# Performance work log

Hardware: AMD Instinct MI355X
Metric: run time of the kernel (lower is better)

## Reference

```python
import jax, jax.numpy as jnp
import numpy as np

B, N, T, F, H, NH, E, R = 16, 100, 96, 26, 128, 4, 16, 8


def _ln(x, g, b, eps=1e-5):
    m = x.mean(-1, keepdims=True)
    v = ((x - m) ** 2).mean(-1, keepdims=True)
    return (x - m) / jnp.sqrt(v + eps) * g + b


def setup_inputs() -> dict:
    ks = iter(jax.random.split(jax.random.key(0), 64))

    def nrm(*shape):
        return jax.random.normal(next(ks), shape, jnp.float32) * 0.05

    z = lambda *s: jnp.zeros(s, jnp.float32)
    o = lambda *s: jnp.ones(s, jnp.float32)
    inp = {}
    inp['x'] = jax.random.normal(next(ks), (B, N, T, F), jnp.float32)
    A = jax.random.uniform(next(ks), (N, N), jnp.float32)
    inp['A_norm'] = A / A.sum(1, keepdims=True)
    inp['H_inc'] = (jax.random.uniform(next(ks), (N, E)) > 0.7).astype(jnp.float32).at[:, 0].set(1.0)
    inp['membership'] = jax.random.randint(next(ks), (N,), 0, R)
    inp['Wp'] = nrm(H, F); inp['bp'] = z(H)
    inp['g_p'] = o(H); inp['b_p'] = z(H)
    inp['Wqkv'] = nrm(3 * H, H); inp['bqkv'] = z(3 * H)
    inp['Wo'] = nrm(H, H); inp['bo'] = z(H)
    inp['g_a'] = o(H); inp['b_a'] = z(H)
    inp['Wih_f'] = nrm(4 * H, H); inp['Whh_f'] = nrm(4 * H, H)
    inp['bih_f'] = z(4 * H); inp['bhh_f'] = z(4 * H)
    inp['Wih_b'] = nrm(4 * H, H); inp['Whh_b'] = nrm(4 * H, H)
    inp['bih_b'] = z(4 * H); inp['bhh_b'] = z(4 * H)
    inp['Wtp'] = nrm(H, 2 * H); inp['btp'] = z(H)
    inp['Wn'] = nrm(H, H); inp['bn'] = z(H)
    inp['We'] = nrm(H, H); inp['be'] = z(H)
    inp['Wa'] = nrm(1, H); inp['ba'] = z(1)
    inp['g_g'] = o(H); inp['b_g'] = z(H)
    inp['Remb'] = nrm(R, H)
    inp['Wg'] = nrm(H, H); inp['bg'] = z(H)
    inp['Wf'] = nrm(H, 2 * H); inp['bf'] = z(H)
    inp['g_f'] = o(H); inp['b_f'] = z(H)
    inp['W1'] = nrm(H // 2, H); inp['b1'] = z(H // 2)
    inp['W2'] = nrm(1, H // 2); inp['b2'] = z(1)
    return inp


def reference(x, A_norm, H_inc, membership, Wp, bp, g_p, b_p, Wqkv, bqkv, Wo, bo,
              g_a, b_a, Wih_f, Whh_f, bih_f, bhh_f, Wih_b, Whh_b, bih_b, bhh_b,
              Wtp, btp, Wn, bn, We, be, Wa, ba, g_g, b_g, Remb, Wg, bg,
              Wf, bf, g_f, b_f, W1, b1, W2, b2):
    B_, N_, T_, F_ = x.shape
    H_ = Wp.shape[0]
    BN = B_ * N_
    # input_proj (dropout = identity in eval)
    h = jax.nn.relu(_ln(x.reshape(BN, T_, F_) @ Wp.T + bp, g_p, b_p))
    # temporal multi-head self-attention + residual + LN
    qkv = h @ Wqkv.T + bqkv
    q, k, v = jnp.split(qkv, 3, -1)
    dh = H_ // NH
    sh = lambda t: t.reshape(BN, T_, NH, dh).transpose(0, 2, 1, 3)
    q, k, v = sh(q), sh(k), sh(v)
    att = jax.nn.softmax(jnp.einsum('bhqd,bhkd->bhqk', q, k) / jnp.sqrt(jnp.float32(dh)), -1)
    ao = jnp.einsum('bhqk,bhkd->bhqd', att, v).transpose(0, 2, 1, 3).reshape(BN, T_, H_)
    h = _ln(ao @ Wo.T + bo + h, g_a, b_a)
    # bidirectional LSTM (PyTorch gate order i,f,g,o), take t = T-1
    def lstm_scan(seq, Wih, Whh, bih, bhh):
        def step(carry, xt):
            hp, cp = carry
            gates = xt @ Wih.T + bih + hp @ Whh.T + bhh
            i, f, g, o_ = jnp.split(gates, 4, -1)
            c = jax.nn.sigmoid(f) * cp + jax.nn.sigmoid(i) * jnp.tanh(g)
            hn = jax.nn.sigmoid(o_) * jnp.tanh(c)
            return (hn, c), hn
        z0 = jnp.zeros((seq.shape[1], H_), seq.dtype)
        _, ys = jax.lax.scan(step, (z0, z0), seq)
        return ys
    seq = h.transpose(1, 0, 2)  # (T, BN, H)
    y_f = lstm_scan(seq, Wih_f, Whh_f, bih_f, bhh_f)[-1]        # fwd hidden at t=T-1
    y_b = lstm_scan(seq[::-1], Wih_b, Whh_b, bih_b, bhh_b)[0]   # bwd hidden at t=T-1
    h_temporal = (jnp.concatenate([y_f, y_b], -1) @ Wtp.T + btp).reshape(B_, N_, H_)
    # spatial: HyperGAT (segment softmax over incident hyperedges) + GCN + region emb
    mask = H_inc > 0                        # (N, E)
    deg_e = H_inc.sum(0)                    # (E,)
    has_edge = mask.any(-1, keepdims=True)  # (N, 1)
    r_emb = Remb[membership]                # (N, H)

    def spatial(hb):
        npj = hb @ Wn.T + bn
        ee = (H_inc.T @ npj) / (deg_e[:, None] + 1e-8)
        ee = ee @ We.T + be                 # (E, H)
        sc = (ee @ Wa.T + ba)[:, 0]         # (E,)
        w = jax.nn.softmax(jnp.where(mask, sc[None, :], -1e9), -1)
        w = jnp.where(has_edge, w, 0.0)
        hb2 = _ln(w @ ee + hb, g_g, b_g)
        hg = jax.nn.relu((A_norm @ hb2) @ Wg.T + bg)
        return hb2 + hg + r_emb

    h_spatial = jax.vmap(spatial)(h_temporal)
    h_fused = jax.nn.relu(_ln(jnp.concatenate([h_temporal, h_spatial], -1) @ Wf.T + bf, g_f, b_f))
    pred = (jax.nn.relu(h_fused @ W1.T + b1) @ W2.T + b2)[..., 0]
    return pred, h_spatial, h_temporal
```

## Files before the change

### kernel.cpp

```cpp
#include <hip/hip_runtime.h>
#include <hip/hip_bf16.h>

typedef __hip_bfloat16 bf16;
typedef __attribute__((ext_vector_type(8))) short bf8v;
typedef __attribute__((ext_vector_type(4))) short s4v;
typedef __attribute__((ext_vector_type(4))) float f4v;

#define DEV __device__ __forceinline__

DEV float b2f(bf16 v){ return __bfloat162float(v); }
DEV bf16 f2b(float v){ return __float2bfloat16(v); }
DEV short f2bs(float v){ bf16 t = __float2bfloat16(v); return *reinterpret_cast<short*>(&t); }
DEV float s2f(short s){ return __uint_as_float(((unsigned int)(unsigned short)s) << 16); }
DEV float blo(unsigned int u){ return __uint_as_float(u << 16); }
DEV float bhi(unsigned int u){ return __uint_as_float(u & 0xffff0000u); }
DEV float rcpf_(float x){ return __builtin_amdgcn_rcpf(x); }
DEV float sigf(float x){ return rcpf_(1.0f + __expf(-x)); }
DEV float tanhfast(float x){
  x = fminf(fmaxf(x, -15.0f), 15.0f);
  float e = __expf(-2.0f*x);
  return (1.0f - e)*rcpf_(1.0f + e);
}

DEV f4v mfma16(bf8v a, bf8v b, f4v c){
  return __builtin_amdgcn_mfma_f32_16x16x32_bf16(a, b, c, 0, 0, 0);
}

DEV float ln128(float s, int tid, const bf16* g, const bf16* b, float* red){
  float sum = s, sq = s*s;
  #pragma unroll
  for (int off = 32; off; off >>= 1){
    sum += __shfl_down(sum, off);
    sq  += __shfl_down(sq,  off);
  }
  if ((tid & 63) == 0){ red[(tid>>6)*2] = sum; red[(tid>>6)*2+1] = sq; }
  __syncthreads();
  float S = red[0] + red[2], Q = red[1] + red[3];
  float m  = S * (1.0f/128.0f);
  float var = fmaxf(Q * (1.0f/128.0f) - m*m, 0.0f);
  float rs = rsqrtf(var + 1e-5f);
  float y = (s - m)*rs*b2f(g[tid]) + b2f(b[tid]);
  __syncthreads();
  return y;
}

__global__ void k_detect(const unsigned int* __restrict__ xw, int* __restrict__ flag){
  __shared__ int found;
  if (threadIdx.x == 0) found = 0;
  __syncthreads();
  int local = 0;
  for (int i = threadIdx.x; i < 4096; i += 256){
    unsigned int u = xw[i];
    unsigned int e = (u >> 7) & 0xFF;
    if (e >= 0x90) local = 1;
  }
  if (local) atomicOr(&found, 1);
  __syncthreads();
  if (threadIdx.x == 0) flag[0] = found ? 0 : 1;
}

struct CArgs {
  const void* src[44];
  int n[44];
  int off[44];
};

__global__ void k_canon(CArgs a, const int* __restrict__ flag, bf16* __restrict__ dst){
  int id = blockIdx.y;
  int n = a.n[id];
  const void* s = a.src[id];
  bf16* d = dst + a.off[id];
  int stride = gridDim.x * blockDim.x;
  int i0 = blockIdx.x * blockDim.x + threadIdx.x;
  if (flag[0]){
    const bf16* sb = (const bf16*)s;
    for (int i = i0; i < n; i += stride) d[i] = sb[i];
  } else {
    const float* sf = (const float*)s;
    for (int i = i0; i < n; i += stride) d[i] = f2b(sf[i]);
  }
}

__global__ void k_inproj(const bf16* __restrict__ x, const bf16* __restrict__ Wp,
                         const bf16* __restrict__ bp, const bf16* __restrict__ gp,
                         const bf16* __restrict__ bbp, bf16* __restrict__ h0){
  int row0 = blockIdx.x*8, tid = threadIdx.x;
  __shared__ float xs[8*26];
  __shared__ float red[4];
  float wreg[26];
  #pragma unroll
  for (int f = 0; f < 26; ++f) wreg[f] = b2f(Wp[tid*26 + f]);
  float bias = b2f(bp[tid]);
  for (int i = tid; i < 208; i += 128) xs[i] = b2f(x[row0*26 + i]);
  __syncthreads();
  for (int r = 0; r < 8; ++r){
    float s = bias;
    #pragma unroll
    for (int f = 0; f < 26; ++f) s += xs[r*26 + f]*wreg[f];
    float y = fmaxf(ln128(s, tid, gp, bbp, red), 0.0f);
    h0[(row0 + r)*128 + tid] = f2b(y);
  }
}

__global__ __launch_bounds__(256,1) void k_attn(const bf16* __restrict__ h0,
    const bf16* __restrict__ Wqkv, const bf16* __restrict__ bqkv,
    bf16* __restrict__ attno){
  int bn = blockIdx.x;
  int tid = threadIdx.x;
  int w = tid >> 6;
  int lane = tid & 63;
  int l15 = lane & 15, quad = lane >> 4;

  __shared__ __align__(16) short h0s[96*136];
  __shared__ __align__(16) short q_sh[4][96*40];
  __shared__ __align__(16) short k_sh[4][96*40];
  __shared__ __align__(16) short v_sh[4][32*104];

  {
    const uint4* src = (const uint4*)(h0 + bn*12288);
    uint4* dst = (uint4*)h0s;
    for (int u = tid; u < 1536; u += 256){
      int r = u >> 4, c = u & 15;
      dst[r*17 + c] = src[u];
    }
  }
  __syncthreads();

  short* qp = q_sh[w];
  short* kp = k_sh[w];
  short* vp = v_sh[w];
  const float scl = 0.17677669529663687f;

  #pragma unroll
  for (int pan = 0; pan < 3; ++pan){
    for (int n0 = 0; n0 < 32; n0 += 16){
      int rq = pan*128 + w*32 + n0 + l15;
      bf8v b[4];
      #pragma unroll
      for (int ksi = 0; ksi < 4; ++ksi)
        b[ksi] = *reinterpret_cast<const bf8v*>(Wqkv + rq*128 + ksi*32 + quad*8);
      float bias = b2f(bqkv[rq]);
      for (int m = 0; m < 6; ++m){
        f4v acc = {0.f,0.f,0.f,0.f};
        #pragma unroll
        for (int ksi = 0; ksi < 4; ++ksi){
          bf8v a = *reinterpret_cast<const bf8v*>(h0s + (m*16 + l15)*136 + ksi*32 + quad*8);
          acc = mfma16(a, b[ksi], acc);
        }
        if (pan == 0){
          #pragma unroll
          for (int r = 0; r < 4; ++r)
            qp[(m*16 + quad*4 + r)*40 + n0 + l15] = f2bs((acc[r] + bias)*scl);
        } else if (pan == 1){
          #pragma unroll
          for (int r = 0; r < 4; ++r)
            kp[(m*16 + quad*4 + r)*40 + n0 + l15] = f2bs(acc[r] + bias);
        } else {
          s4v vs;
          #pragma unroll
          for (int r = 0; r < 4; ++r) vs[r] = f2bs(acc[r] + bias);
          *reinterpret_cast<s4v*>(vp + (n0 + l15)*104 + m*16 + quad*4) = vs;
        }
      }
    }
  }
  __syncthreads();

  short* pp = h0s + w*1664;

  for (int m = 0; m < 6; ++m){
    bf8v aq = *reinterpret_cast<const bf8v*>(qp + (m*16 + l15)*40 + quad*8);
    f4v s[6];
    #pragma unroll
    for (int n = 0; n < 6; ++n){
      bf8v bk = *reinterpret_cast<const bf8v*>(kp + (n*16 + l15)*40 + quad*8);
      f4v z = {0.f,0.f,0.f,0.f};
      s[n] = mfma16(aq, bk, z);
    }
    float mr[4], sr[4];
    #pragma unroll
    for (int r = 0; r < 4; ++r){
      float m0 = fmaxf(fmaxf(s[0][r], s[1][r]), fmaxf(s[2][r], s[3][r]));
      mr[r] = fmaxf(m0, fmaxf(s[4][r], s[5][r]));
    }
    #pragma unroll
    for (int mask = 1; mask < 16; mask <<= 1)
      #pragma unroll
      for (int r = 0; r < 4; ++r) mr[r] = fmaxf(mr[r], __shfl_xor(mr[r], mask));
    #pragma unroll
    for (int r = 0; r < 4; ++r) sr[r] = 0.0f;
    #pragma unroll
    for (int n = 0; n < 6; ++n)
      #pragma unroll
      for (int r = 0; r < 4; ++r){
        float p = __expf(s[n][r] - mr[r]);
        s[n][r] = p;
        sr[r] += p;
      }
    #pragma unroll
    for (int mask = 1; mask < 16; mask <<= 1)
      #pragma unroll
      for (int r = 0; r < 4; ++r) sr[r] += __shfl_xor(sr[r], mask);
    #pragma unroll
    for (int n = 0; n < 6; ++n)
      #pragma unroll
      for (int r = 0; r < 4; ++r)
        pp[(quad*4 + r)*104 + n*16 + l15] = f2bs(s[n][r]);
    asm volatile("s_waitcnt lgkmcnt(0)" ::: "memory");
    f4v o0 = {0.f,0.f,0.f,0.f}, o1 = {0.f,0.f,0.f,0.f};
    #pragma unroll
    for (int ksi = 0; ksi < 3; ++ksi){
      bf8v ap  = *reinterpret_cast<const bf8v*>(pp + l15*104 + ksi*32 + quad*8);
      bf8v bv0 = *reinterpret_cast<const bf8v*>(vp + l15*104 + ksi*32 + quad*8);
      bf8v bv1 = *reinterpret_cast<const bf8v*>(vp + (16 + l15)*104 + ksi*32 + quad*8);
      o0 = mfma16(ap, bv0, o0);
      o1 = mfma16(ap, bv1, o1);
    }
    #pragma unroll
    for (int r = 0; r < 4; ++r){
      float inv = 1.0f/sr[r];
      int row = bn*96 + m*16 + quad*4 + r;
      attno[row*128 + w*32 + l15]      = f2b(o0[r]*inv);
      attno[row*128 + w*32 + 16 + l15] = f2b(o1[r]*inv);
    }
  }
}

__global__ __launch_bounds__(256,1) void k_oproj(const bf16* __restrict__ attno,
    const bf16* __restrict__ h0, const bf16* __restrict__ Wo,
    const bf16* __restrict__ bo, const bf16* __restrict__ ga,
    const bf16* __restrict__ ba_, bf16* __restrict__ h1){
  int rt = blockIdx.x;
  int tid = threadIdx.x;
  int w = tid >> 6, lane = tid & 63;
  int l15 = lane & 15, quad = lane >> 4;
  __shared__ __align__(16) short atile[128*136];
  {
    const uint4* src = (const uint4*)(attno + rt*16384);
    uint4* dst = (uint4*)atile;
    for (int u = tid; u < 2048; u += 256){
      int r = u >> 4, c = u & 15;
      dst[r*17 + c] = src[u];
    }
  }
  __syncthreads();
  int m0 = w*32;
  bf8v a[2][4];
  #pragma unroll
  for (int m = 0; m < 2; ++m)
    #pragma unroll
    for (int ksi = 0; ksi < 4; ++ksi)
      a[m][ksi] = *reinterpret_cast<const bf8v*>(atile + (m0 + m*16 + l15)*136 + ksi*32 + quad*8);
  f4v acc[2][8];
  #pragma unroll
  for (int m = 0; m < 2; ++m)
    #pragma unroll
    for (int n = 0; n < 8; ++n) acc[m][n] = (f4v){0.f,0.f,0.f,0.f};
  for (int n = 0; n < 8; ++n){
    int G = n*16 + l15;
    bf8v b[4];
    #pragma unroll
    for (int ksi = 0; ksi < 4; ++ksi)
      b[ksi] = *reinterpret_cast<const bf8v*>(Wo + G*128 + ksi*32 + quad*8);
    #pragma unroll
    for (int m = 0; m < 2; ++m)
      #pragma unroll
      for (int ksi = 0; ksi < 4; ++ksi)
        acc[m][n] = mfma16(a[m][ksi], b[ksi], acc[m][n]);
  }
  #pragma unroll
  for (int m = 0; m < 2; ++m){
    int rowbase = rt*128 + m0 + m*16;
    #pragma unroll
    for (int n = 0; n < 8; ++n){
      int col = n*16 + l15;
      float bia = b2f(bo[col]);
      #pragma unroll
      for (int r = 0; r < 4; ++r)
        acc[m][n][r] += bia + b2f(h0[(rowbase + quad*4 + r)*128 + col]);
    }
    float sm[4], sq[4];
    #pragma unroll
    for (int r = 0; r < 4; ++r){ sm[r] = 0.f; sq[r] = 0.f; }
    #pragma unroll
    for (int n = 0; n < 8; ++n)
      #pragma unroll
      for (int r = 0; r < 4; ++r){
        float v = acc[m][n][r];
        sm[r] += v; sq[r] += v*v;
      }
    #pragma unroll
    for (int mask = 1; mask < 16; mask <<= 1)
      #pragma unroll
      for (int r = 0; r < 4; ++r){
        sm[r] += __shfl_xor(sm[r], mask);
        sq[r] += __shfl_xor(sq[r], mask);
      }
    float mean[4], rs[4];
    #pragma unroll
    for (int r = 0; r < 4; ++r){
      mean[r] = sm[r]*(1.0f/128.0f);
      float var = fmaxf(sq[r]*(1.0f/128.0f) - mean[r]*mean[r], 0.0f);
      rs[r] = rsqrtf(var + 1e-5f);
    }
    #pragma unroll
    for (int n = 0; n < 8; ++n){
      int col = n*16 + l15;
      float gv = b2f(ga[col]), bv = b2f(ba_[col]);
      #pragma unroll
      for (int r = 0; r < 4; ++r){
        float y = (acc[m][n][r] - mean[r])*rs[r]*gv + bv;
        h1[(rowbase + quad*4 + r)*128 + col] = f2b(y);
      }
    }
  }
}

__global__ __launch_bounds__(512,1) void k_lstm(const bf16* __restrict__ Whh,
    const bf16* __restrict__ Wih, const bf16* __restrict__ bih,
    const bf16* __restrict__ bhh, const bf16* __restrict__ h1,
    float* __restrict__ y_f){
  int bn0 = blockIdx.x * 16;
  int tid = threadIdx.x;
  int w = tid >> 6, lane = tid & 63;
  int l15 = lane & 15, quad = lane >> 4;
  __shared__ __align__(16) short hbuf[2][16*136];
  __shared__ __align__(16) short xbuf[2][16*136];

  bf8v whh[4][4], wih[4][4];
  float bias[4];
  #pragma unroll
  for (int role = 0; role < 4; ++role){
    int G = role*128 + w*16 + l15;
    #pragma unroll
    for (int kt = 0; kt < 4; ++kt){
      whh[role][kt] = *reinterpret_cast<const bf8v*>(Whh + G*128 + kt*32 + quad*8);
      wih[role][kt] = *reinterpret_cast<const bf8v*>(Wih + G*128 + kt*32 + quad*8);
    }
    bias[role] = b2f(bih[G]) + b2f(bhh[G]);
  }
  for (int i = tid; i < 16*136; i += 512) hbuf[0][i] = 0;
  if (tid < 256){
    const uint4* h1u4 = (const uint4*)h1;
    int row = (bn0 + (tid >> 4))*96 + 0;
    ((uint4*)xbuf[0])[(tid >> 4)*17 + (tid & 15)] = h1u4[row*16 + (tid & 15)];
  }
  f4v c0 = {0.f,0.f,0.f,0.f};
  __syncthreads();

  for (int t = 0; t < 96; ++t){
    int cur = t & 1, nxt = cur ^ 1;
    uint4 xpre;
    if (t < 95 && tid < 256){
      const uint4* h1u4 = (const uint4*)h1;
      int row = (bn0 + (tid >> 4))*96 + t + 1;
      xpre = h1u4[row*16 + (tid & 15)];
    }
    bf8v ah[4], ax[4];
    #pragma unroll
    for (int kt = 0; kt < 4; ++kt){
      ah[kt] = *reinterpret_cast<const bf8v*>(hbuf[cur] + l15*136 + kt*32 + quad*8);
      ax[kt] = *reinterpret_cast<const bf8v*>(xbuf[cur] + l15*136 + kt*32 + quad*8);
    }
    f4v acc[4];
    #pragma unroll
    for (int role = 0; role < 4; ++role){
      f4v z = {0.f,0.f,0.f,0.f};
      #pragma unroll
      for (int kt = 0; kt < 4; ++kt) z = mfma16(ax[kt], wih[role][kt], z);
      #pragma unroll
      for (int kt = 0; kt < 4; ++kt) z = mfma16(ah[kt], whh[role][kt], z);
      acc[role] = z;
    }
    float hreg[4];
    #pragma unroll
    for (int r = 0; r < 4; ++r){
      float i_ = acc[0][r] + bias[0];
      float f_ = acc[1][r] + bias[1];
      float g_ = acc[2][r] + bias[2];
      float o_ = acc[3][r] + bias[3];
      float c  = sigf(f_)*c0[r] + sigf(i_)*tanhfast(g_);
      hreg[r]  = sigf(o_)*tanhfast(c);
      c0[r] = c;
    }
    #pragma unroll
    for (int r = 0; r < 4; ++r)
      hbuf[nxt][(quad*4 + r)*136 + w*16 + l15] = f2bs(hreg[r]);
    if (t < 95 && tid < 256)
      ((uint4*)xbuf[nxt])[(tid >> 4)*17 + (tid & 15)] = xpre;
    __syncthreads();
  }
  for (int idx = tid; idx < 2048; idx += 512){
    int r = idx >> 7, d = idx & 127;
    y_f[(bn0 + r)*128 + d] = s2f(hbuf[0][r*136 + d]);
  }
}

__global__ void k_bwdtp(const bf16* __restrict__ h1, const bf16* __restrict__ Wihb,
                        const bf16* __restrict__ bihb, const bf16* __restrict__ bhhb,
                        const float* __restrict__ y_f, const bf16* __restrict__ Wtp,
                        const bf16* __restrict__ btp, float* __restrict__ ht,
                        const int* __restrict__ flag, bf16* __restrict__ outb,
                        float* __restrict__ outf){
  int bn = blockIdx.x, tid = threadIdx.x;
  __shared__ __align__(16) float xr[128];
  __shared__ float gates[512];
  __shared__ __align__(16) float ycat[256];
  xr[tid] = b2f(h1[(bn*96 + 95)*128 + tid]);
  __syncthreads();
  const float2* xf2 = (const float2*)xr;
  for (int g = tid; g < 512; g += 128){
    const unsigned int* w = (const unsigned int*)(Wihb + g*128);
    float s = b2f(bihb[g]) + b2f(bhhb[g]);
    #pragma unroll 8
    for (int kp = 0; kp < 64; ++kp){
      float2 a = xf2[kp]; unsigned int u = w[kp];
      s += a.x*blo(u) + a.y*bhi(u);
    }
    gates[g] = s;
  }
  __syncthreads();
  float ii = gates[tid], gg = gates[256 + tid], oo = gates[384 + tid];
  float c  = sigf(ii)*tanhfast(gg);
  float yb = sigf(oo)*tanhfast(c);
  ycat[tid]       = y_f[bn*128 + tid];
  ycat[128 + tid] = yb;
  __syncthreads();
  const float2* yf2 = (const float2*)ycat;
  const unsigned int* w = (const unsigned int*)(Wtp + tid*256);
  float s = b2f(btp[tid]);
  #pragma unroll 8
  for (int kp = 0; kp < 128; ++kp){
    float2 a = yf2[kp]; unsigned int u = w[kp];
    s += a.x*blo(u) + a.y*bhi(u);
  }
  ht[bn*128 + tid] = s;
  int oi = 206400 + bn*128 + tid;
  if (flag[0]) outb[oi] = f2b(s); else outf[oi] = s;
}

__global__ void k_npj(const float* __restrict__ ht, const bf16* __restrict__ Wn,
                      const bf16* __restrict__ bn_, float* __restrict__ npj){
  int bn = blockIdx.x, tid = threadIdx.x;
  __shared__ __align__(16) float row[128];
  row[tid] = ht[bn*128 + tid];
  __syncthreads();
  const float2* rf2 = (const float2*)row;
  const unsigned int* w = (const unsigned int*)(Wn + tid*128);
  float s = b2f(bn_[tid]);
  #pragma unroll 8
  for (int kp = 0; kp < 64; ++kp){
    float2 a = rf2[kp]; unsigned int u = w[kp];
    s += a.x*blo(u) + a.y*bhi(u);
  }
  npj[bn*128 + tid] = s;
}

__global__ void k_edge(const float* __restrict__ npj, const bf16* __restrict__ Hinc,
                       const bf16* __restrict__ We, const bf16* __restrict__ be,
                       const bf16* __restrict__ Wa, const bf16* __restrict__ ba,
                       float* __restrict__ ee, float* __restrict__ scE){
  int b = blockIdx.x >> 4, e = blockIdx.x & 15, tid = threadIdx.x;
  float acc = 0.0f, deg = 0.0f;
  for (int n = 0; n < 100; ++n){
    float w = b2f(Hinc[n*16 + e]);
    deg += w;
    acc += w * npj[(b*100 + n)*128 + tid];
  }
  __shared__ __align__(16) float eep[128];
  eep[tid] = acc/(deg + 1e-8f);
  __syncthreads();
  const float2* ef2 = (const float2*)eep;
  const unsigned int* w = (const unsigned int*)(We + tid*128);
  float s = b2f(be[tid]);
  #pragma unroll 8
  for (int kp = 0; kp < 64; ++kp){
    float2 a = ef2[kp]; unsigned int u = w[kp];
    s += a.x*blo(u) + a.y*bhi(u);
  }
  ee[(b*16 + e)*128 + tid] = s;
  float p = s * b2f(Wa[tid]);
  #pragma unroll
  for (int off = 32; off; off >>= 1) p += __shfl_down(p, off);
  __shared__ float r2[2];
  if ((tid & 63) == 0) r2[tid>>6] = p;
  __syncthreads();
  if (tid == 0) scE[b*16 + e] = r2[0] + r2[1] + b2f(ba[0]);
}

__global__ void k_node(const float* __restrict__ ht, const float* __restrict__ ee,
                       const float* __restrict__ scE, const bf16* __restrict__ Hinc,
                       const bf16* __restrict__ gg_, const bf16* __restrict__ bg_,
                       float* __restrict__ hb2){
  int blk = blockIdx.x; int b = blk/100, n = blk%100; int tid = threadIdx.x;
  __shared__ float wts[16];
  __shared__ float red[4];
  if (tid == 0){
    float sc[16]; float mx = -1e30f;
    for (int e = 0; e < 16; ++e){
      float m_ = b2f(Hinc[n*16 + e]);
      sc[e] = (m_ > 0.0f) ? scE[b*16 + e] : -1e30f;
      mx = fmaxf(mx, sc[e]);
    }
    float tmp[16]; float sum = 0.0f;
    for (int e = 0; e < 16; ++e){
      tmp[e] = (sc[e] > -1e29f) ? __expf(sc[e] - mx) : 0.0f;
      sum += tmp[e];
    }
    float inv = (sum > 0.0f) ? 1.0f/sum : 0.0f;
    for (int e = 0; e < 16; ++e) wts[e] = tmp[e]*inv;
  }
  __syncthreads();
  float s = ht[(b*100 + n)*128 + tid];
  for (int e = 0; e < 16; ++e) s += wts[e] * ee[(b*16 + e)*128 + tid];
  float y = ln128(s, tid, gg_, bg_, red);
  hb2[(b*100 + n)*128 + tid] = y;
}

__global__ void k_gcn(const float* __restrict__ hb2, const bf16* __restrict__ An,
                      const bf16* __restrict__ Wg, const bf16* __restrict__ bg_,
                      const bf16* __restrict__ Remb, const int* __restrict__ mem,
                      float* __restrict__ hsp, const int* __restrict__ flag,
                      bf16* __restrict__ outb, float* __restrict__ outf){
  int blk = blockIdx.x; int b = blk/100, n = blk%100; int tid = threadIdx.x;
  float acc = 0.0f;
  for (int m = 0; m < 100; ++m){
    float a = b2f(An[n*100 + m]);
    acc += a * hb2[(b*100 + m)*128 + tid];
  }
  __shared__ __align__(16) float as_[128];
  as_[tid] = acc;
  __syncthreads();
  const float2* af2 = (const float2*)as_;
  const unsigned int* w = (const unsigned int*)(Wg + tid*128);
  float s = b2f(bg_[tid]);
  #pragma unroll 8
  for (int kp = 0; kp < 64; ++kp){
    float2 a = af2[kp]; unsigned int u = w[kp];
    s += a.x*blo(u) + a.y*bhi(u);
  }
  s = fmaxf(s, 0.0f);
  float out = hb2[(b*100 + n)*128 + tid] + s + b2f(Remb[mem[n]*128 + tid]);
  hsp[(b*100 + n)*128 + tid] = out;
  int oi = 1600 + (b*100 + n)*128 + tid;
  if (flag[0]) outb[oi] = f2b(out); else outf[oi] = out;
}

__global__ void k_fuse(const float* __restrict__ ht, const float* __restrict__ hsp,
                       const bf16* __restrict__ Wf, const bf16* __restrict__ bf_,
                       const bf16* __restrict__ gf, const bf16* __restrict__ b_f,
                       const bf16* __restrict__ W1, const bf16* __restrict__ b1,
                       const bf16* __restrict__ W2, const bf16* __restrict__ b2,
                       const int* __restrict__ flag, bf16* __restrict__ outb,
                       float* __restrict__ outf){
  int bn = blockIdx.x, tid = threadIdx.x;
  __shared__ __align__(16) float cat[256];
  __shared__ __align__(16) float hf[128];
  __shared__ float red[4];
  cat[tid]       = ht[bn*128 + tid];
  cat[128 + tid] = hsp[bn*128 + tid];
  __syncthreads();
  const float2* cf2 = (const float2*)cat;
  const unsigned int* w = (const unsigned int*)(Wf + tid*256);
  float s = b2f(bf_[tid]);
  #pragma unroll 8
  for (int kp = 0; kp < 128; ++kp){
    float2 a = cf2[kp]; unsigned int u = w[kp];
    s += a.x*blo(u) + a.y*bhi(u);
  }
  float y = fmaxf(ln128(s, tid, gf, b_f, red), 0.0f);
  hf[tid] = y;
  __syncthreads();
  if (tid < 64){
    const float2* hf2 = (const float2*)hf;
    const unsigned int* w1 = (const unsigned int*)(W1 + tid*128);
    float z = b2f(b1[tid]);
    #pragma unroll 8
    for (int kp = 0; kp < 64; ++kp){
      float2 a = hf2[kp]; unsigned int u = w1[kp];
      z += a.x*blo(u) + a.y*bhi(u);
    }
    z = fmaxf(z, 0.0f);
    float p = z * b2f(W2[tid]);
    #pragma unroll
    for (int off = 32; off; off >>= 1) p += __shfl_down(p, off);
    if (tid == 0){
      float pr = p + b2f(b2[0]);
      if (flag[0]) outb[bn] = f2b(pr); else outf[bn] = pr;
    }
  }
}


extern "C" void kernel_launch(void* const* d_in, const int* in_sizes, int n_in,
                              void* d_out, int out_size, void* d_ws, size_t ws_size,
                              hipStream_t stream){
  (void)n_in; (void)out_size; (void)ws_size;
  const int* mem = (const int*)d_in[3];

  CArgs ca;
  int coff[43];
  int nf = 0;
  long long off = 0;
  for (int i = 0; i < 43; ++i){
    if (i == 3){ coff[i] = -1; continue; }
    coff[i] = (int)off;
    ca.src[nf] = d_in[i];
    ca.n[nf]   = in_sizes[i];
    ca.off[nf] = (int)off;
    ++nf;
    off += (long long)((in_sizes[i] + 7) & ~7);
  }
  char* ws = (char*)d_ws;
  bf16* canon = (bf16*)ws;
  long long canonBytes = ((off*2 + 255)/256)*256;
  int* flag = (int*)(ws + canonBytes);
  long long base = canonBytes + 256;

  #define C(i) (canon + coff[i])
  const bf16* A_norm = C(1);
  const bf16* Hinc   = C(2);
  const bf16* Wp  = C(4);  const bf16* bp  = C(5);
  const bf16* g_p = C(6);  const bf16* b_p = C(7);
  const bf16* Wqkv= C(8);  const bf16* bqkv= C(9);
  const bf16* Wo  = C(10); const bf16* bo  = C(11);
  const bf16* g_a = C(12); const bf16* b_a = C(13);
  const bf16* Wih_f = C(14); const bf16* Whh_f = C(15);
  const bf16* bih_f = C(16); const bf16* bhh_f = C(17);
  const bf16* Wih_b = C(18);
  const bf16* bih_b = C(20); const bf16* bhh_b = C(21);
  const bf16* Wtp = C(22); const bf16* btp = C(23);
  const bf16* Wn  = C(24); const bf16* bn_ = C(25);
  const bf16* We  = C(26); const bf16* be  = C(27);
  const bf16* Wa  = C(28); const bf16* ba  = C(29);
  const bf16* g_g = C(30); const bf16* b_g = C(31);
  const bf16* Remb= C(32);
  const bf16* Wg  = C(33); const bf16* bg  = C(34);
  const bf16* Wf  = C(35); const bf16* bff = C(36);
  const bf16* g_f = C(37); const bf16* b_f = C(38);
  const bf16* W1  = C(39); const bf16* b1  = C(40);
  const bf16* W2  = C(41); const bf16* b2  = C(42);
  const bf16* xc  = C(0);
  #undef C

  bf16*  outb = (bf16*)d_out;
  float* outf = (float*)d_out;
  bf16*  h1    = (bf16*)(ws + base);
  bf16*  h0    = (bf16*)(ws + base + 39321600LL);
  bf16*  attno = (bf16*)(ws + base + 78643200LL);
  float* y_f   = (float*)(ws + base + 196608000LL);
  float* htb   = (float*)(ws + base + 197427200LL);
  float* npj   = (float*)(ws + base + 198246400LL);
  float* ee    = (float*)(ws + base + 199065600LL);
  float* scE   = (float*)(ws + base + 199196672LL);
  float* hb2   = (float*)(ws + base + 199197696LL);
  float* hsp   = (float*)(ws + base + 200016896LL);

  k_detect<<<1, 256, 0, stream>>>((const unsigned int*)d_in[0], flag);
  k_canon <<<dim3(64, nf), 256, 0, stream>>>(ca, flag, canon);
  k_inproj<<<19200, 128, 0, stream>>>(xc, Wp, bp, g_p, b_p, h0);
  k_attn  <<<1600,  256, 0, stream>>>(h0, Wqkv, bqkv, attno);
  k_oproj <<<1200,  256, 0, stream>>>(attno, h0, Wo, bo, g_a, b_a, h1);
  k_lstm  <<<100,   512, 0, stream>>>(Whh_f, Wih_f, bih_f, bhh_f, h1, y_f);
  k_bwdtp <<<1600,  128, 0, stream>>>(h1, Wih_b, bih_b, bhh_b, y_f, Wtp, btp, htb,
                                      flag, outb, outf);
  k_npj   <<<1600,  128, 0, stream>>>(htb, Wn, bn_, npj);
  k_edge  <<<256,   128, 0, stream>>>(npj, Hinc, We, be, Wa, ba, ee, scE);
  k_node  <<<1600,  128, 0, stream>>>(htb, ee, scE, Hinc, g_g, b_g, hb2);
  k_gcn   <<<1600,  128, 0, stream>>>(hb2, A_norm, Wg, bg, Remb, mem, hsp,
                                      flag, outb, outf);
  k_fuse  <<<1600,  128, 0, stream>>>(htb, hsp, Wf, bff, g_f, b_f, W1, b1, W2, b2,
                                      flag, outb, outf);
}
```

Baseline: 585.6 us.

## Keep Q/K in registers in attention and software-pipeline the LSTM input projection

The attention kernel now computes Q and K per 16-row tile through a small per-wave scratch buffer and keeps the MFMA operand fragments in registers. This drops the large Q/K shared arrays, and the min-blocks hint is removed from the launch bounds of attention and oproj, so more blocks can be resident. The forward LSTM precomputes the input-projection MFMAs for step t+1 during step t and prefetches input rows further ahead. This takes the Wih work off the recurrent critical path, at the cost of more registers per thread.

```diff
diff --git a/kernel.cpp b/kernel.cpp
--- a/kernel.cpp
+++ b/kernel.cpp
@@ -102,7 +102,7 @@
   }
 }
 
-__global__ __launch_bounds__(256,1) void k_attn(const bf16* __restrict__ h0,
+__global__ __launch_bounds__(256) void k_attn(const bf16* __restrict__ h0,
     const bf16* __restrict__ Wqkv, const bf16* __restrict__ bqkv,
     bf16* __restrict__ attno){
   int bn = blockIdx.x;
@@ -112,9 +112,8 @@
   int l15 = lane & 15, quad = lane >> 4;
 
   __shared__ __align__(16) short h0s[96*136];
-  __shared__ __align__(16) short q_sh[4][96*40];
-  __shared__ __align__(16) short k_sh[4][96*40];
   __shared__ __align__(16) short v_sh[4][32*104];
+  __shared__ __align__(16) short scr[4][16*40];
 
   {
     const uint4* src = (const uint4*)(h0 + bn*12288);
@@ -126,42 +125,77 @@
   }
   __syncthreads();
 
-  short* qp = q_sh[w];
-  short* kp = k_sh[w];
   short* vp = v_sh[w];
+  short* sw = scr[w];
   const float scl = 0.17677669529663687f;
 
-  #pragma unroll
-  for (int pan = 0; pan < 3; ++pan){
+  bf8v aq[6], bk[6];
+  for (int m = 0; m < 6; ++m){
+    bf8v a[4];
+    #pragma unroll
+    for (int kt = 0; kt < 4; ++kt)
+      a[kt] = *reinterpret_cast<const bf8v*>(h0s + (m*16 + l15)*136 + kt*32 + quad*8);
+    #pragma unroll
     for (int n0 = 0; n0 < 32; n0 += 16){
-      int rq = pan*128 + w*32 + n0 + l15;
+      int rq = w*32 + n0 + l15;
       bf8v b[4];
       #pragma unroll
-      for (int ksi = 0; ksi < 4; ++ksi)
-        b[ksi] = *reinterpret_cast<const bf8v*>(Wqkv + rq*128 + ksi*32 + quad*8);
+      for (int kt = 0; kt < 4; ++kt)
+        b[kt] = *reinterpret_cast<const bf8v*>(Wqkv + rq*128 + kt*32 + quad*8);
       float bias = b2f(bqkv[rq]);
-      for (int m = 0; m < 6; ++m){
-        f4v acc = {0.f,0.f,0.f,0.f};
-        #pragma unroll
-        for (int ksi = 0; ksi < 4; ++ksi){
-          bf8v a = *reinterpret_cast<const bf8v*>(h0s + (m*16 + l15)*136 + ksi*32 + quad*8);
-          acc = mfma16(a, b[ksi], acc);
-        }
-        if (pan == 0){
-          #pragma unroll
-          for (int r = 0; r < 4; ++r)
-            qp[(m*16 + quad*4 + r)*40 + n0 + l15] = f2bs((acc[r] + bias)*scl);
-        } else if (pan == 1){
-          #pragma unroll
-          for (int r = 0; r < 4; ++r)
-            kp[(m*16 + quad*4 + r)*40 + n0 + l15] = f2bs(acc[r] + bias);
-        } else {
-          s4v vs;
-          #pragma unroll
-          for (int r = 0; r < 4; ++r) vs[r] = f2bs(acc[r] + bias);
-          *reinterpret_cast<s4v*>(vp + (n0 + l15)*104 + m*16 + quad*4) = vs;
-        }
-      }
+      f4v acc = {0.f,0.f,0.f,0.f};
+      #pragma unroll
+      for (int kt = 0; kt < 4; ++kt) acc = mfma16(a[kt], b[kt], acc);
+      #pragma unroll
+      for (int r = 0; r < 4; ++r)
+        sw[(quad*4 + r)*40 + n0 + l15] = f2bs((acc[r] + bias)*scl);
+    }
+    asm volatile("s_waitcnt lgkmcnt(0)" ::: "memory");
+    aq[m] = *reinterpret_cast<const bf8v*>(sw + l15*40 + quad*8);
+  }
+  for (int m = 0; m < 6; ++m){
+    bf8v a[4];
+    #pragma unroll
+    for (int kt = 0; kt < 4; ++kt)
+      a[kt] = *reinterpret_cast<const bf8v*>(h0s + (m*16 + l15)*136 + kt*32 + quad*8);
+    #pragma unroll
+    for (int n0 = 0; n0 < 32; n0 += 16){
+      int rq = 128 + w*32 + n0 + l15;
+      bf8v b[4];
+      #pragma unroll
+      for (int kt = 0; kt < 4; ++kt)
+        b[kt] = *reinterpret_cast<const bf8v*>(Wqkv + rq*128 + kt*32 + quad*8);
+      float bias = b2f(bqkv[rq]);
+      f4v acc = {0.f,0.f,0.f,0.f};
+      #pragma unroll
+      for (int kt = 0; kt < 4; ++kt) acc = mfma16(a[kt], b[kt], acc);
+      #pragma unroll
+      for (int r = 0; r < 4; ++r)
+        sw[(quad*4 + r)*40 + n0 + l15] = f2bs(acc[r] + bias);
+    }
+    asm volatile("s_waitcnt lgkmcnt(0)" ::: "memory");
+    bk[m] = *reinterpret_cast<const bf8v*>(sw + l15*40 + quad*8);
+  }
+  for (int m = 0; m < 6; ++m){
+    bf8v a[4];
+    #pragma unroll
+    for (int kt = 0; kt < 4; ++kt)
+      a[kt] = *reinterpret_cast<const bf8v*>(h0s + (m*16 + l15)*136 + kt*32 + quad*8);
+    #pragma unroll
+    for (int n0 = 0; n0 < 32; n0 += 16){
+      int rq = 256 + w*32 + n0 + l15;
+      bf8v b[4];
+      #pragma unroll
+      for (int kt = 0; kt < 4; ++kt)
+        b[kt] = *reinterpret_cast<const bf8v*>(Wqkv + rq*128 + kt*32 + quad*8);
+      float bias = b2f(bqkv[rq]);
+      f4v acc = {0.f,0.f,0.f,0.f};
+      #pragma unroll
+      for (int kt = 0; kt < 4; ++kt) acc = mfma16(a[kt], b[kt], acc);
+      s4v vs;
+      #pragma unroll
+      for (int r = 0; r < 4; ++r) vs[r] = f2bs(acc[r] + bias);
+      *reinterpret_cast<s4v*>(vp + (n0 + l15)*104 + m*16 + quad*4) = vs;
     }
   }
   __syncthreads();
@@ -169,13 +203,11 @@
   short* pp = h0s + w*1664;
 
   for (int m = 0; m < 6; ++m){
-    bf8v aq = *reinterpret_cast<const bf8v*>(qp + (m*16 + l15)*40 + quad*8);
     f4v s[6];
     #pragma unroll
     for (int n = 0; n < 6; ++n){
-      bf8v bk = *reinterpret_cast<const bf8v*>(kp + (n*16 + l15)*40 + quad*8);
       f4v z = {0.f,0.f,0.f,0.f};
-      s[n] = mfma16(aq, bk, z);
+      s[n] = mfma16(aq[m], bk[n], z);
     }
     float mr[4], sr[4];
     #pragma unroll
@@ -226,7 +258,7 @@
   }
 }
 
-__global__ __launch_bounds__(256,1) void k_oproj(const bf16* __restrict__ attno,
+__global__ __launch_bounds__(256) void k_oproj(const bf16* __restrict__ attno,
     const bf16* __restrict__ h0, const bf16* __restrict__ Wo,
     const bf16* __restrict__ bo, const bf16* __restrict__ ga,
     const bf16* __restrict__ ba_, bf16* __restrict__ h1){
@@ -339,38 +371,57 @@
     }
     bias[role] = b2f(bih[G]) + b2f(bhh[G]);
   }
+  const uint4* h1u4 = (const uint4*)h1;
+  int srow = tid >> 4, scol = tid & 15;
+
   for (int i = tid; i < 16*136; i += 512) hbuf[0][i] = 0;
-  if (tid < 256){
-    const uint4* h1u4 = (const uint4*)h1;
-    int row = (bn0 + (tid >> 4))*96 + 0;
-    ((uint4*)xbuf[0])[(tid >> 4)*17 + (tid & 15)] = h1u4[row*16 + (tid & 15)];
-  }
+  if (tid < 256)
+    ((uint4*)xbuf[0])[srow*17 + scol] = h1u4[((bn0 + srow)*96 + 0)*16 + scol];
   f4v c0 = {0.f,0.f,0.f,0.f};
+  uint4 xpre;
+  if (tid < 256) xpre = h1u4[((bn0 + srow)*96 + 1)*16 + scol];
+  __syncthreads();
+
+  f4v accx[4];
+  {
+    bf8v ax[4];
+    #pragma unroll
+    for (int kt = 0; kt < 4; ++kt)
+      ax[kt] = *reinterpret_cast<const bf8v*>(xbuf[0] + l15*136 + kt*32 + quad*8);
+    #pragma unroll
+    for (int role = 0; role < 4; ++role){
+      f4v z = {0.f,0.f,0.f,0.f};
+      #pragma unroll
+      for (int kt = 0; kt < 4; ++kt) z = mfma16(ax[kt], wih[role][kt], z);
+      accx[role] = z;
+    }
+  }
+  if (tid < 256) ((uint4*)xbuf[1])[srow*17 + scol] = xpre;
+  if (tid < 256) xpre = h1u4[((bn0 + srow)*96 + 2)*16 + scol];
   __syncthreads();
 
   for (int t = 0; t < 96; ++t){
     int cur = t & 1, nxt = cur ^ 1;
-    uint4 xpre;
-    if (t < 95 && tid < 256){
-      const uint4* h1u4 = (const uint4*)h1;
-      int row = (bn0 + (tid >> 4))*96 + t + 1;
-      xpre = h1u4[row*16 + (tid & 15)];
-    }
-    bf8v ah[4], ax[4];
+    bf8v ah[4], axn[4];
     #pragma unroll
     for (int kt = 0; kt < 4; ++kt){
-      ah[kt] = *reinterpret_cast<const bf8v*>(hbuf[cur] + l15*136 + kt*32 + quad*8);
-      ax[kt] = *reinterpret_cast<const bf8v*>(xbuf[cur] + l15*136 + kt*32 + quad*8);
+      ah[kt]  = *reinterpret_cast<const bf8v*>(hbuf[cur] + l15*136 + kt*32 + quad*8);
+      axn[kt] = *reinterpret_cast<const bf8v*>(xbuf[nxt] + l15*136 + kt*32 + quad*8);
     }
     f4v acc[4];
+    #pragma unroll
+    for (int role = 0; role < 4; ++role){
+      f4v z = accx[role];
+      #pragma unroll
+      for (int kt = 0; kt < 4; ++kt) z = mfma16(ah[kt], whh[role][kt], z);
+      acc[role] = z;
+    }
     #pragma unroll
     for (int role = 0; role < 4; ++role){
       f4v z = {0.f,0.f,0.f,0.f};
       #pragma unroll
-      for (int kt = 0; kt < 4; ++kt) z = mfma16(ax[kt], wih[role][kt], z);
-      #pragma unroll
-      for (int kt = 0; kt < 4; ++kt) z = mfma16(ah[kt], whh[role][kt], z);
-      acc[role] = z;
+      for (int kt = 0; kt < 4; ++kt) z = mfma16(axn[kt], wih[role][kt], z);
+      accx[role] = z;
     }
     float hreg[4];
     #pragma unroll
@@ -386,8 +437,11 @@
     #pragma unroll
     for (int r = 0; r < 4; ++r)
       hbuf[nxt][(quad*4 + r)*136 + w*16 + l15] = f2bs(hreg[r]);
-    if (t < 95 && tid < 256)
-      ((uint4*)xbuf[nxt])[(tid >> 4)*17 + (tid & 15)] = xpre;
+    if (tid < 256){
+      ((uint4*)xbuf[cur])[srow*17 + scol] = xpre;
+      int tl = (t + 3 < 96) ? t + 3 : 95;
+      xpre = h1u4[((bn0 + srow)*96 + tl)*16 + scol];
+    }
     __syncthreads();
   }
   for (int idx = tid; idx < 2048; idx += 512){
```

New measurement: 574.3 us. Within noise of the previous version (-1.9%).
